# Optimization experiments

Hardware: AMD Instinct MI355X
Metric: run time of the kernel (lower is better)

## Reference

```python
import jax, jax.numpy as jnp
import numpy as np

L, H, W, C = 5, 32, 128, 256
HEADS, DH = 8, 32
NUM_TYPES, NUM_REL = 2, 4
INNER = HEADS * DH  # 256
LN_EPS = 1e-5


def setup_inputs() -> dict:
    key = jax.random.key(0)
    ks = jax.random.split(key, 16)
    s = 0.05
    x = jax.random.normal(ks[0], (L, H, W, C), jnp.float32)
    mask = jax.random.randint(ks[1], (H, W, 1, L), 0, 2).astype(jnp.int32)
    types = jax.random.randint(ks[2], (L,), 0, NUM_TYPES)
    # prior_encoding carries the node type in channel 2 (constant across H,W)
    prior_encoding = jnp.zeros((L, H, W, 3), jnp.float32)
    prior_encoding = prior_encoding.at[:, :, :, 2].set(
        jnp.broadcast_to(types[:, None, None].astype(jnp.float32), (L, H, W)))
    return {
        'x': x,
        'mask': mask,
        'prior_encoding': prior_encoding,
        'ln_gamma': jnp.ones((C,), jnp.float32),
        'ln_beta': jnp.zeros((C,), jnp.float32),
        'q_weight': jax.random.normal(ks[3], (NUM_TYPES, INNER, C), jnp.float32) * s,
        'q_bias': jnp.zeros((NUM_TYPES, INNER), jnp.float32),
        'k_weight': jax.random.normal(ks[4], (NUM_TYPES, INNER, C), jnp.float32) * s,
        'k_bias': jnp.zeros((NUM_TYPES, INNER), jnp.float32),
        'v_weight': jax.random.normal(ks[5], (NUM_TYPES, INNER, C), jnp.float32) * s,
        'v_bias': jnp.zeros((NUM_TYPES, INNER), jnp.float32),
        'a_weight': jax.random.normal(ks[6], (NUM_TYPES, C, INNER), jnp.float32) * s,
        'a_bias': jnp.zeros((NUM_TYPES, C), jnp.float32),
        'relation_att': jax.random.normal(ks[7], (NUM_REL, HEADS, DH, DH), jnp.float32) * s,
        'relation_msg': jax.random.normal(ks[8], (NUM_REL, HEADS, DH, DH), jnp.float32) * s,
    }


def reference(x, mask, prior_encoding, ln_gamma, ln_beta,
              q_weight, q_bias, k_weight, k_bias, v_weight, v_bias,
              a_weight, a_bias, relation_att, relation_msg):
    # --- prenorm (LayerNorm over last dim), x: (L,H,W,C) ---
    mu = jnp.mean(x, axis=-1, keepdims=True)
    var = jnp.mean(jnp.square(x - mu), axis=-1, keepdims=True)
    xn = (x - mu) * jax.lax.rsqrt(var + LN_EPS) * ln_gamma + ln_beta

    xh = jnp.transpose(xn, (1, 2, 0, 3))  # (H,W,L,C)
    types = prior_encoding[:, 0, 0, 2].astype(jnp.int32)
    types = jnp.clip(types, 0, None)  # (L,)
    n_types = q_weight.shape[0]
    heads, dh = relation_att.shape[1], relation_att.shape[2]
    Hh, Ww, Ll = xh.shape[0], xh.shape[1], xh.shape[2]

    def type_linear(w, b):  # per-token typed projection
        return jnp.einsum('hwlc,lic->hwli', xh, w[types]) + b[types]

    def to_heads(t):  # (H,W,L,inner) -> (m,H,W,L,dh)
        return jnp.transpose(t.reshape(Hh, Ww, Ll, heads, dh), (3, 0, 1, 2, 4))

    q = to_heads(type_linear(q_weight, q_bias))
    k = to_heads(type_linear(k_weight, k_bias))
    v = to_heads(type_linear(v_weight, v_bias))

    # per-edge relation matrices: rel_idx (L,L)
    rel_idx = types[:, None] * n_types + types[None, :]
    w_att = jnp.transpose(relation_att[rel_idx], (2, 0, 1, 3, 4))  # (m,L,L,dh,dh)
    w_msg = jnp.transpose(relation_msg[rel_idx], (2, 0, 1, 3, 4))  # (m,L,L,dh,dh)

    scale = jnp.asarray(dh, jnp.float32) ** -0.5
    # att_map = (q @ w_att) @ k^T, per (head, h, w, i, j)
    att = jnp.einsum('mhwip,mijpq,mhwjq->mhwij', q, w_att, k) * scale
    att = jnp.where(mask[None] == 0, jnp.float32(-1e9), att)  # mask: (1,H,W,1,L)
    att = jax.nn.softmax(att, axis=-1)

    # out = att @ (w_msg @ v)
    out = jnp.einsum('mhwij,mijpc,mhwjp->mhwic', att, w_msg, v)  # (m,H,W,L,dh)
    out = jnp.transpose(out, (1, 2, 3, 0, 4)).reshape(Hh, Ww, Ll, heads * dh)

    # typed output projection back to C
    out = jnp.einsum('hwli,lci->hwlc', out, a_weight[types]) + a_bias[types]
    return jnp.transpose(out, (2, 0, 1, 3))  # (L,H,W,C)
```

## Files before the change

### kernel.cpp

```cpp
#include <hip/hip_runtime.h>
#include <math.h>

#define LL 5
#define HH 32
#define WW 128
#define CC 256
#define HEADS 8
#define DHH 32
#define HW (HH*WW)
#define NTOK (LL*HW)
#define LN_EPS 1e-5f

typedef short bf16x8 __attribute__((ext_vector_type(8)));
typedef float f32x4 __attribute__((ext_vector_type(4)));
typedef unsigned short u16x8 __attribute__((ext_vector_type(8)));

__device__ __forceinline__ int clamp01(int t) { return t < 0 ? 0 : (t > 1 ? 1 : t); }

__device__ __forceinline__ unsigned short f2b(float f) {
    union { float f; unsigned u; } v; v.f = f;
    unsigned r = v.u + 0x7FFFu + ((v.u >> 16) & 1u);
    return (unsigned short)(r >> 16);
}
__device__ __forceinline__ float b2f(unsigned short u) {
    union { unsigned u; float f; } v; v.u = ((unsigned)u) << 16; return v.f;
}

__device__ __forceinline__ size_t frag_off(int row, int col) {
    return ((size_t)((row >> 4) * 8 + (col >> 5)) << 9)
         + (((col & 31) >> 3) << 7) + ((row & 15) << 3) + (col & 7);
}

__global__ __launch_bounds__(256) void setup_kernel(
        const float* __restrict__ x, const float* __restrict__ g, const float* __restrict__ b,
        unsigned short* __restrict__ xn,
        const float* __restrict__ qw, const float* __restrict__ aw,
        unsigned short* __restrict__ qwb, unsigned short* __restrict__ awb,
        const float* __restrict__ relA, const float* __restrict__ relM,
        const float* __restrict__ kw, const float* __restrict__ vw,
        const float* __restrict__ kb, const float* __restrict__ vb,
        unsigned short* __restrict__ wattb, unsigned short* __restrict__ wmsgb,
        float* __restrict__ batt, float* __restrict__ bmsg) {
    __shared__ float Bl[32][256];
    int blk = blockIdx.x;
    int wave = threadIdx.x >> 6, lane = threadIdx.x & 63;
    if (blk < 1280) {
        float4 gv = *(const float4*)(g + lane * 4);
        float4 bv = *(const float4*)(b + lane * 4);
        #pragma unroll
        for (int rr = 0; rr < 4; ++rr) {
            int row = blk * 16 + wave * 4 + rr;
            const float4 xv = *(const float4*)(x + (size_t)row * CC + lane * 4);
            float s1 = xv.x + xv.y + xv.z + xv.w;
            float s2 = xv.x * xv.x + xv.y * xv.y + xv.z * xv.z + xv.w * xv.w;
            #pragma unroll
            for (int off = 32; off; off >>= 1) {
                s1 += __shfl_xor(s1, off, 64);
                s2 += __shfl_xor(s2, off, 64);
            }
            float mu = s1 * (1.0f / CC);
            float inv = rsqrtf(s2 * (1.0f / CC) - mu * mu + LN_EPS);
            ushort4 o;
            o.x = f2b((xv.x - mu) * inv * gv.x + bv.x);
            o.y = f2b((xv.y - mu) * inv * gv.y + bv.y);
            o.z = f2b((xv.z - mu) * inv * gv.z + bv.z);
            o.w = f2b((xv.w - mu) * inv * gv.w + bv.w);
            *(ushort4*)(xn + frag_off(row, lane << 2)) = o;
        }
    } else if (blk < 1408) {
        int task = (blk - 1280) * 4 + wave;
        int mtx = task >> 8, rem = task & 255;
        int t = rem >> 7, panel = (rem >> 3) & 15, kk = rem & 7;
        const float* S = (mtx ? aw : qw) + (size_t)t * 65536
                       + (size_t)(panel * 16 + (lane & 15)) * 256 + kk * 32 + (lane >> 4) * 8;
        float4 f0 = *(const float4*)S;
        float4 f1 = *(const float4*)(S + 4);
        u16x8 o;
        o[0] = f2b(f0.x); o[1] = f2b(f0.y); o[2] = f2b(f0.z); o[3] = f2b(f0.w);
        o[4] = f2b(f1.x); o[5] = f2b(f1.y); o[6] = f2b(f1.z); o[7] = f2b(f1.w);
        unsigned short* D = (mtx ? awb : qwb) + (size_t)t * 65536
                          + (((size_t)(panel * 8 + kk)) << 9) + (lane << 3);
        *(u16x8*)D = o;
    } else {
        int fb = blk - 1408;
        int r = fb & 3, m = (fb >> 2) & 7, which = fb >> 5;
        int tsel = r & 1;
        const float* S  = (which ? relM : relA) + ((size_t)r * 8 + m) * 1024;
        const float* Bg = (which ? vw : kw) + (size_t)tsel * 65536 + (size_t)m * 32 * 256;
        const float* bv = (which ? vb : kb) + tsel * 256 + m * 32;
        unsigned short* Wf = (which ? wmsgb : wattb) + (size_t)r * 65536;
        float* bo = (which ? bmsg : batt) + r * 256 + m * 32;

        for (int i = threadIdx.x; i < 32 * 256; i += 256)
            Bl[i >> 8][i & 255] = Bg[(size_t)(i >> 8) * 256 + (i & 255)];
        __syncthreads();

        int a  = threadIdx.x >> 3;
        int c0 = (threadIdx.x & 7) * 4;
        float srow[32];
        #pragma unroll
        for (int bq = 0; bq < 32; ++bq)
            srow[bq] = which ? S[bq * 32 + a] : S[a * 32 + bq];
        float acc[8][4] = {{0.f}};
        #pragma unroll
        for (int bq = 0; bq < 32; ++bq) {
            float s = srow[bq];
            #pragma unroll
            for (int cc = 0; cc < 8; ++cc) {
                float4 bb = *(const float4*)&Bl[bq][c0 + cc * 32];
                acc[cc][0] += s * bb.x; acc[cc][1] += s * bb.y;
                acc[cc][2] += s * bb.z; acc[cc][3] += s * bb.w;
            }
        }
        int colpanel = m * 2 + (a >> 4);
        int jr = a & 15;
        #pragma unroll
        for (int cc = 0; cc < 8; ++cc) {
            ushort4 w4;
            w4.x = f2b(acc[cc][0]); w4.y = f2b(acc[cc][1]);
            w4.z = f2b(acc[cc][2]); w4.w = f2b(acc[cc][3]);
            *(ushort4*)(Wf + (((size_t)(colpanel * 8 + cc)) << 9)
                           + ((c0 >> 3) << 7) + (jr << 3) + (c0 & 7)) = w4;
        }
        if (threadIdx.x < 32) {
            int p = threadIdx.x;
            float s = 0.f;
            #pragma unroll
            for (int bq = 0; bq < 32; ++bq)
                s += (which ? S[bq * 32 + p] : S[p * 32 + bq]) * bv[bq];
            bo[p] = s;
        }
    }
}

__global__ __launch_bounds__(256) void gemm_qkv(const short* __restrict__ X,
        const short* __restrict__ qwb, const short* __restrict__ wattb,
        const short* __restrict__ wmsgb,
        const float* __restrict__ qb, const float* __restrict__ batt,
        const float* __restrict__ bmsg,
        const float* __restrict__ prior, unsigned short* __restrict__ OutBase) {
    __shared__ float R[4][16][68];
    int blkrow = blockIdx.x * 32;
    int s = blockIdx.y;
    int l = blkrow >> 12;
    int t = clamp01((int)prior[(size_t)l * HW * 3 + 2]);

    const short* Wp; const float* Bp;
    if (s == 0)      { Wp = qwb   + (size_t)t * 65536;                          Bp = qb   + t * 256; }
    else if (s <= 2) { int i2 = (s - 1) * 2 + t; Wp = wattb + (size_t)i2 * 65536; Bp = batt + i2 * 256; }
    else             { int i2 = (s - 3) * 2 + t; Wp = wmsgb + (size_t)i2 * 65536; Bp = bmsg + i2 * 256; }
    unsigned short* Out = OutBase + (size_t)s * NTOK * 256;

    int wave = threadIdx.x >> 6, lane = threadIdx.x & 63;
    int lr = lane & 15;
    const short* Xf = X + ((size_t)blockIdx.x << 13);

    f32x4 acc[2][4];
    #pragma unroll
    for (int mr = 0; mr < 2; ++mr)
        #pragma unroll
        for (int nr = 0; nr < 4; ++nr) acc[mr][nr] = (f32x4){0.f, 0.f, 0.f, 0.f};

    #pragma unroll
    for (int kk = 0; kk < 8; ++kk) {
        bf16x8 af[2], bf[4];
        #pragma unroll
        for (int mr = 0; mr < 2; ++mr)
            af[mr] = *(const bf16x8*)(Xf + (((size_t)(mr * 8 + kk)) << 9) + (lane << 3));
        #pragma unroll
        for (int nr = 0; nr < 4; ++nr)
            bf[nr] = *(const bf16x8*)(Wp + (((size_t)((wave * 4 + nr) * 8 + kk)) << 9) + (lane << 3));
        #pragma unroll
        for (int mr = 0; mr < 2; ++mr)
            #pragma unroll
            for (int nr = 0; nr < 4; ++nr)
                acc[mr][nr] = __builtin_amdgcn_mfma_f32_16x16x32_bf16(af[mr], bf[nr], acc[mr][nr], 0, 0, 0);
    }

    float bias[4];
    #pragma unroll
    for (int nr = 0; nr < 4; ++nr) bias[nr] = Bp[wave * 64 + nr * 16 + lr];

    int q = lane >> 4;
    int c8 = lane & 7;
    #pragma unroll
    for (int mr = 0; mr < 2; ++mr) {
        #pragma unroll
        for (int nr = 0; nr < 4; ++nr)
            #pragma unroll
            for (int rr = 0; rr < 4; ++rr)
                R[wave][q * 4 + rr][nr * 16 + lr] = acc[mr][nr][rr] + bias[nr];
        #pragma unroll
        for (int p = 0; p < 2; ++p) {
            int r = (lane >> 3) + p * 8;
            float4 v0 = *(const float4*)&R[wave][r][c8 * 8];
            float4 v1 = *(const float4*)&R[wave][r][c8 * 8 + 4];
            u16x8 w;
            w[0] = f2b(v0.x); w[1] = f2b(v0.y); w[2] = f2b(v0.z); w[3] = f2b(v0.w);
            w[4] = f2b(v1.x); w[5] = f2b(v1.y); w[6] = f2b(v1.z); w[7] = f2b(v1.w);
            *(u16x8*)(Out + (size_t)(blkrow + mr * 16 + r) * 256 + wave * 64 + c8 * 8) = w;
        }
        __builtin_amdgcn_wave_barrier();
    }
}

__global__ __launch_bounds__(256) void attn_proj(
        const unsigned short* __restrict__ QKV, const short* __restrict__ awb,
        const float* __restrict__ ab, const int* __restrict__ mask,
        const float* __restrict__ prior, float* __restrict__ out) {
    __shared__ unsigned short Att[32 * 256];
    const size_t TSTR = (size_t)NTOK * 256;
    int tid = threadIdx.x;
    int blkrow = blockIdx.x * 32;
    int i = blkrow >> 12;
    int t = clamp01((int)prior[(size_t)i * HW * 3 + 2]);

    int tok = tid >> 3, m = tid & 7;
    int row = blkrow + tok;
    int hw = row & (HW - 1);

    {
        const unsigned short* Qp = QKV + (size_t)row * 256 + m * 32;
        const unsigned short* Kb = QKV + (size_t)(1 + t) * TSTR + (size_t)hw * 256 + m * 32;
        const unsigned short* Vb = QKV + (size_t)(3 + t) * TSTR + (size_t)hw * 256 + m * 32;

        float qf[32];
        #pragma unroll
        for (int c = 0; c < 4; ++c) {
            bf16x8 qv = *(const bf16x8*)(Qp + c * 8);
            #pragma unroll
            for (int e = 0; e < 8; ++e) qf[c * 8 + e] = b2f((unsigned short)qv[e]);
        }

        const float scale = 0.17677669529663687f;
        float s[LL];
        #pragma unroll
        for (int j = 0; j < LL; ++j) {
            const unsigned short* Kp = Kb + (size_t)j * HW * 256;
            float acc = 0.f;
            #pragma unroll
            for (int c = 0; c < 4; ++c) {
                bf16x8 kv = *(const bf16x8*)(Kp + c * 8);
                #pragma unroll
                for (int e = 0; e < 8; ++e)
                    acc = fmaf(qf[c * 8 + e], b2f((unsigned short)kv[e]), acc);
            }
            int mk = mask[hw * LL + j];
            s[j] = mk ? acc * scale : -1e9f;
        }

        float mx = fmaxf(fmaxf(fmaxf(s[0], s[1]), fmaxf(s[2], s[3])), s[4]);
        float e5[LL], sum = 0.f;
        #pragma unroll
        for (int j = 0; j < LL; ++j) { e5[j] = __expf(s[j] - mx); sum += e5[j]; }
        float inv = 1.f / sum;

        float o[32];
        #pragma unroll
        for (int c = 0; c < 32; ++c) o[c] = 0.f;
        #pragma unroll
        for (int j = 0; j < LL; ++j) {
            const unsigned short* Vp = Vb + (size_t)j * HW * 256;
            float ej = e5[j];
            #pragma unroll
            for (int c = 0; c < 4; ++c) {
                bf16x8 vv = *(const bf16x8*)(Vp + c * 8);
                #pragma unroll
                for (int e = 0; e < 8; ++e)
                    o[c * 8 + e] = fmaf(ej, b2f((unsigned short)vv[e]), o[c * 8 + e]);
            }
        }

        int panel = tok >> 4, tr = tok & 15;
        #pragma unroll
        for (int c8 = 0; c8 < 4; ++c8) {
            u16x8 w;
            #pragma unroll
            for (int e = 0; e < 8; ++e) w[e] = f2b(o[c8 * 8 + e] * inv);
            *(u16x8*)(&Att[((panel * 8 + m) << 9) + c8 * 128 + tr * 8]) = w;
        }
    }
    __syncthreads();

    int wave = tid >> 6, lane = tid & 63, lr = lane & 15;
    const short* Wp = awb + (size_t)t * 65536;
    const float* Bp = ab + (size_t)t * 256;

    f32x4 acc[2][4];
    #pragma unroll
    for (int mr = 0; mr < 2; ++mr)
        #pragma unroll
        for (int nr = 0; nr < 4; ++nr) acc[mr][nr] = (f32x4){0.f, 0.f, 0.f, 0.f};

    #pragma unroll
    for (int kk = 0; kk < 8; ++kk) {
        bf16x8 af[2], bf[4];
        #pragma unroll
        for (int mr = 0; mr < 2; ++mr)
            af[mr] = *(const bf16x8*)((const short*)Att + ((mr * 8 + kk) << 9) + (lane << 3));
        #pragma unroll
        for (int nr = 0; nr < 4; ++nr)
            bf[nr] = *(const bf16x8*)(Wp + (((size_t)((wave * 4 + nr) * 8 + kk)) << 9) + (lane << 3));
        #pragma unroll
        for (int mr = 0; mr < 2; ++mr)
            #pragma unroll
            for (int nr = 0; nr < 4; ++nr)
                acc[mr][nr] = __builtin_amdgcn_mfma_f32_16x16x32_bf16(af[mr], bf[nr], acc[mr][nr], 0, 0, 0);
    }

    #pragma unroll
    for (int nr = 0; nr < 4; ++nr) {
        int col = wave * 64 + nr * 16 + lr;
        float bias = Bp[col];
        #pragma unroll
        for (int mr = 0; mr < 2; ++mr) {
            #pragma unroll
            for (int rr = 0; rr < 4; ++rr) {
                int orow = blkrow + mr * 16 + (lane >> 4) * 4 + rr;
                out[(size_t)orow * 256 + col] = acc[mr][nr][rr] + bias;
            }
        }
    }
}

extern "C" void kernel_launch(void* const* d_in, const int* in_sizes, int n_in,
                              void* d_out, int out_size, void* d_ws, size_t ws_size,
                              hipStream_t stream) {
    (void)in_sizes; (void)n_in; (void)out_size; (void)ws_size;
    const float* x     = (const float*)d_in[0];
    const int*   mask  = (const int*)d_in[1];
    const float* prior = (const float*)d_in[2];
    const float* ln_g  = (const float*)d_in[3];
    const float* ln_b  = (const float*)d_in[4];
    const float* qw    = (const float*)d_in[5];
    const float* qb    = (const float*)d_in[6];
    const float* kw    = (const float*)d_in[7];
    const float* kb    = (const float*)d_in[8];
    const float* vw    = (const float*)d_in[9];
    const float* vb    = (const float*)d_in[10];
    const float* aw    = (const float*)d_in[11];
    const float* ab    = (const float*)d_in[12];
    const float* relA  = (const float*)d_in[13];
    const float* relM  = (const float*)d_in[14];
    float* out = (float*)d_out;

    char* ws = (char*)d_ws;
    const size_t TOKB = (size_t)NTOK * 256 * 2;
    unsigned short* xnb  = (unsigned short*)(ws);
    unsigned short* Qb   = (unsigned short*)(ws + TOKB);
    char* wsp = ws + 6 * TOKB;
    unsigned short* qwb   = (unsigned short*)(wsp);            wsp += 131072 * 2;
    unsigned short* awb   = (unsigned short*)(wsp);            wsp += 131072 * 2;
    unsigned short* wattb = (unsigned short*)(wsp);            wsp += 4 * 65536 * 2;
    unsigned short* wmsgb = (unsigned short*)(wsp);            wsp += 4 * 65536 * 2;
    float* batt = (float*)(wsp);                               wsp += 4 * 256 * 4;
    float* bmsg = (float*)(wsp);

    setup_kernel<<<1472, 256, 0, stream>>>(x, ln_g, ln_b, xnb, qw, aw, qwb, awb,
                                           relA, relM, kw, vw, kb, vb,
                                           wattb, wmsgb, batt, bmsg);

    gemm_qkv<<<dim3(NTOK / 32, 5), 256, 0, stream>>>((const short*)xnb,
            (const short*)qwb, (const short*)wattb, (const short*)wmsgb,
            qb, batt, bmsg, prior, Qb);

    attn_proj<<<NTOK / 32, 256, 0, stream>>>(Qb, (const short*)awb, ab, mask, prior, out);
}
```

Before: 64.49 us.

## Keep weight fragments in registers and loop over eight row panels per block

The QKV GEMM kernel now loads its 64-column weight slice into registers once per wave and reuses it across eight 16-row panels, instead of reloading weights for every 32-row block. The grid shrinks from 640 to 160 blocks per projection, and launch bounds request two blocks per SIMD. This is meant to cut repeated weight traffic from L2 and the per-block setup cost. In exchange it uses many more VGPRs for the 32 held weight fragments, which may cause spills, and the smaller grid (800 blocks total) lowers parallelism.

```diff
diff --git a/kernel.cpp b/kernel.cpp
--- a/kernel.cpp
+++ b/kernel.cpp
@@ -133,16 +133,18 @@
     }
 }
 
-__global__ __launch_bounds__(256) void gemm_qkv(const short* __restrict__ X,
+__global__ __launch_bounds__(256, 2) void gemm_qkv(const short* __restrict__ X,
         const short* __restrict__ qwb, const short* __restrict__ wattb,
         const short* __restrict__ wmsgb,
         const float* __restrict__ qb, const float* __restrict__ batt,
         const float* __restrict__ bmsg,
         const float* __restrict__ prior, unsigned short* __restrict__ OutBase) {
     __shared__ float R[4][16][68];
-    int blkrow = blockIdx.x * 32;
+    int chunk = blockIdx.x;
+    int l = chunk >> 5;
+    int base_panel = l * 256 + (chunk & 31) * 8;
+    int base_row = base_panel << 4;
     int s = blockIdx.y;
-    int l = blkrow >> 12;
     int t = clamp01((int)prior[(size_t)l * HW * 3 + 2]);
 
     const short* Wp; const float* Bp;
@@ -153,29 +155,13 @@
 
     int wave = threadIdx.x >> 6, lane = threadIdx.x & 63;
     int lr = lane & 15;
-    const short* Xf = X + ((size_t)blockIdx.x << 13);
-
-    f32x4 acc[2][4];
-    #pragma unroll
-    for (int mr = 0; mr < 2; ++mr)
-        #pragma unroll
-        for (int nr = 0; nr < 4; ++nr) acc[mr][nr] = (f32x4){0.f, 0.f, 0.f, 0.f};
-
-    #pragma unroll
-    for (int kk = 0; kk < 8; ++kk) {
-        bf16x8 af[2], bf[4];
-        #pragma unroll
-        for (int mr = 0; mr < 2; ++mr)
-            af[mr] = *(const bf16x8*)(Xf + (((size_t)(mr * 8 + kk)) << 9) + (lane << 3));
-        #pragma unroll
-        for (int nr = 0; nr < 4; ++nr)
-            bf[nr] = *(const bf16x8*)(Wp + (((size_t)((wave * 4 + nr) * 8 + kk)) << 9) + (lane << 3));
-        #pragma unroll
-        for (int mr = 0; mr < 2; ++mr)
-            #pragma unroll
-            for (int nr = 0; nr < 4; ++nr)
-                acc[mr][nr] = __builtin_amdgcn_mfma_f32_16x16x32_bf16(af[mr], bf[nr], acc[mr][nr], 0, 0, 0);
-    }
+
+    bf16x8 bf[4][8];
+    #pragma unroll
+    for (int nr = 0; nr < 4; ++nr)
+        #pragma unroll
+        for (int kk = 0; kk < 8; ++kk)
+            bf[nr][kk] = *(const bf16x8*)(Wp + (((size_t)((wave * 4 + nr) * 8 + kk)) << 9) + (lane << 3));
 
     float bias[4];
     #pragma unroll
@@ -183,22 +169,37 @@
 
     int q = lane >> 4;
     int c8 = lane & 7;
-    #pragma unroll
-    for (int mr = 0; mr < 2; ++mr) {
+
+    for (int p = 0; p < 8; ++p) {
+        const short* Ap = X + (((size_t)(base_panel + p)) << 12);
+        bf16x8 af[8];
+        #pragma unroll
+        for (int kk = 0; kk < 8; ++kk)
+            af[kk] = *(const bf16x8*)(Ap + (kk << 9) + (lane << 3));
+
+        f32x4 acc[4];
+        #pragma unroll
+        for (int nr = 0; nr < 4; ++nr) acc[nr] = (f32x4){0.f, 0.f, 0.f, 0.f};
+        #pragma unroll
+        for (int kk = 0; kk < 8; ++kk)
+            #pragma unroll
+            for (int nr = 0; nr < 4; ++nr)
+                acc[nr] = __builtin_amdgcn_mfma_f32_16x16x32_bf16(af[kk], bf[nr][kk], acc[nr], 0, 0, 0);
+
         #pragma unroll
         for (int nr = 0; nr < 4; ++nr)
             #pragma unroll
             for (int rr = 0; rr < 4; ++rr)
-                R[wave][q * 4 + rr][nr * 16 + lr] = acc[mr][nr][rr] + bias[nr];
-        #pragma unroll
-        for (int p = 0; p < 2; ++p) {
-            int r = (lane >> 3) + p * 8;
+                R[wave][q * 4 + rr][nr * 16 + lr] = acc[nr][rr] + bias[nr];
+        #pragma unroll
+        for (int ph = 0; ph < 2; ++ph) {
+            int r = (lane >> 3) + ph * 8;
             float4 v0 = *(const float4*)&R[wave][r][c8 * 8];
             float4 v1 = *(const float4*)&R[wave][r][c8 * 8 + 4];
             u16x8 w;
             w[0] = f2b(v0.x); w[1] = f2b(v0.y); w[2] = f2b(v0.z); w[3] = f2b(v0.w);
             w[4] = f2b(v1.x); w[5] = f2b(v1.y); w[6] = f2b(v1.z); w[7] = f2b(v1.w);
-            *(u16x8*)(Out + (size_t)(blkrow + mr * 16 + r) * 256 + wave * 64 + c8 * 8) = w;
+            *(u16x8*)(Out + (size_t)(base_row + p * 16 + r) * 256 + wave * 64 + c8 * 8) = w;
         }
         __builtin_amdgcn_wave_barrier();
     }
@@ -360,7 +361,7 @@
                                            relA, relM, kw, vw, kb, vb,
                                            wattb, wmsgb, batt, bmsg);
 
-    gemm_qkv<<<dim3(NTOK / 32, 5), 256, 0, stream>>>((const short*)xnb,
+    gemm_qkv<<<dim3(160, 5), 256, 0, stream>>>((const short*)xnb,
             (const short*)qwb, (const short*)wattb, (const short*)wmsgb,
             qb, batt, bmsg, prior, Qb);
 
```

New measurement: 78.10 us. 21.1% more time.

## Split QKV GEMM column halves across blocks and halve attn_proj tile rows

Applied to the files above, without the earlier changes.

The QKV GEMM grid doubles in y so each block computes only half of the 256 output columns, which cuts per-wave accumulators and the staging buffer. The attention/projection kernel now handles 16 tokens per block with 128 threads, and each of its two waves covers 128 output columns. Both changes raise block count and occupancy and lower register pressure. The cost is that X tiles are reloaded twice in the GEMM and each projection weight tile is reused across fewer rows.

```diff
diff --git a/kernel.cpp b/kernel.cpp
--- a/kernel.cpp
+++ b/kernel.cpp
@@ -139,9 +139,9 @@
         const float* __restrict__ qb, const float* __restrict__ batt,
         const float* __restrict__ bmsg,
         const float* __restrict__ prior, unsigned short* __restrict__ OutBase) {
-    __shared__ float R[4][16][68];
+    __shared__ float R[4][16][36];
     int blkrow = blockIdx.x * 32;
-    int s = blockIdx.y;
+    int s = blockIdx.y >> 1, nh = blockIdx.y & 1;
     int l = blkrow >> 12;
     int t = clamp01((int)prior[(size_t)l * HW * 3 + 2]);
 
@@ -154,64 +154,61 @@
     int wave = threadIdx.x >> 6, lane = threadIdx.x & 63;
     int lr = lane & 15;
     const short* Xf = X + ((size_t)blockIdx.x << 13);
-
-    f32x4 acc[2][4];
+    int cpb = nh * 8 + wave * 2;
+
+    f32x4 acc[2][2];
     #pragma unroll
     for (int mr = 0; mr < 2; ++mr)
         #pragma unroll
-        for (int nr = 0; nr < 4; ++nr) acc[mr][nr] = (f32x4){0.f, 0.f, 0.f, 0.f};
+        for (int nr = 0; nr < 2; ++nr) acc[mr][nr] = (f32x4){0.f, 0.f, 0.f, 0.f};
 
     #pragma unroll
     for (int kk = 0; kk < 8; ++kk) {
-        bf16x8 af[2], bf[4];
+        bf16x8 af[2], bf[2];
         #pragma unroll
         for (int mr = 0; mr < 2; ++mr)
             af[mr] = *(const bf16x8*)(Xf + (((size_t)(mr * 8 + kk)) << 9) + (lane << 3));
         #pragma unroll
-        for (int nr = 0; nr < 4; ++nr)
-            bf[nr] = *(const bf16x8*)(Wp + (((size_t)((wave * 4 + nr) * 8 + kk)) << 9) + (lane << 3));
+        for (int nr = 0; nr < 2; ++nr)
+            bf[nr] = *(const bf16x8*)(Wp + (((size_t)((cpb + nr) * 8 + kk)) << 9) + (lane << 3));
         #pragma unroll
         for (int mr = 0; mr < 2; ++mr)
             #pragma unroll
-            for (int nr = 0; nr < 4; ++nr)
+            for (int nr = 0; nr < 2; ++nr)
                 acc[mr][nr] = __builtin_amdgcn_mfma_f32_16x16x32_bf16(af[mr], bf[nr], acc[mr][nr], 0, 0, 0);
     }
 
-    float bias[4];
-    #pragma unroll
-    for (int nr = 0; nr < 4; ++nr) bias[nr] = Bp[wave * 64 + nr * 16 + lr];
+    float bias[2];
+    #pragma unroll
+    for (int nr = 0; nr < 2; ++nr) bias[nr] = Bp[nh * 128 + wave * 32 + nr * 16 + lr];
 
     int q = lane >> 4;
-    int c8 = lane & 7;
     #pragma unroll
     for (int mr = 0; mr < 2; ++mr) {
         #pragma unroll
-        for (int nr = 0; nr < 4; ++nr)
+        for (int nr = 0; nr < 2; ++nr)
             #pragma unroll
             for (int rr = 0; rr < 4; ++rr)
                 R[wave][q * 4 + rr][nr * 16 + lr] = acc[mr][nr][rr] + bias[nr];
-        #pragma unroll
-        for (int p = 0; p < 2; ++p) {
-            int r = (lane >> 3) + p * 8;
-            float4 v0 = *(const float4*)&R[wave][r][c8 * 8];
-            float4 v1 = *(const float4*)&R[wave][r][c8 * 8 + 4];
-            u16x8 w;
-            w[0] = f2b(v0.x); w[1] = f2b(v0.y); w[2] = f2b(v0.z); w[3] = f2b(v0.w);
-            w[4] = f2b(v1.x); w[5] = f2b(v1.y); w[6] = f2b(v1.z); w[7] = f2b(v1.w);
-            *(u16x8*)(Out + (size_t)(blkrow + mr * 16 + r) * 256 + wave * 64 + c8 * 8) = w;
-        }
+        int r = lane >> 2, c8 = lane & 3;
+        float4 v0 = *(const float4*)&R[wave][r][c8 * 8];
+        float4 v1 = *(const float4*)&R[wave][r][c8 * 8 + 4];
+        u16x8 w;
+        w[0] = f2b(v0.x); w[1] = f2b(v0.y); w[2] = f2b(v0.z); w[3] = f2b(v0.w);
+        w[4] = f2b(v1.x); w[5] = f2b(v1.y); w[6] = f2b(v1.z); w[7] = f2b(v1.w);
+        *(u16x8*)(Out + (size_t)(blkrow + mr * 16 + r) * 256 + nh * 128 + wave * 32 + c8 * 8) = w;
         __builtin_amdgcn_wave_barrier();
     }
 }
 
-__global__ __launch_bounds__(256) void attn_proj(
+__global__ __launch_bounds__(128) void attn_proj(
         const unsigned short* __restrict__ QKV, const short* __restrict__ awb,
         const float* __restrict__ ab, const int* __restrict__ mask,
         const float* __restrict__ prior, float* __restrict__ out) {
-    __shared__ unsigned short Att[32 * 256];
+    __shared__ unsigned short Att[16 * 256];
     const size_t TSTR = (size_t)NTOK * 256;
     int tid = threadIdx.x;
-    int blkrow = blockIdx.x * 32;
+    int blkrow = blockIdx.x * 16;
     int i = blkrow >> 12;
     int t = clamp01((int)prior[(size_t)i * HW * 3 + 2]);
 
@@ -271,13 +268,12 @@
             }
         }
 
-        int panel = tok >> 4, tr = tok & 15;
         #pragma unroll
         for (int c8 = 0; c8 < 4; ++c8) {
             u16x8 w;
             #pragma unroll
             for (int e = 0; e < 8; ++e) w[e] = f2b(o[c8 * 8 + e] * inv);
-            *(u16x8*)(&Att[((panel * 8 + m) << 9) + c8 * 128 + tr * 8]) = w;
+            *(u16x8*)(&Att[(m << 9) + c8 * 128 + tok * 8]) = w;
         }
     }
     __syncthreads();
@@ -286,39 +282,28 @@
     const short* Wp = awb + (size_t)t * 65536;
     const float* Bp = ab + (size_t)t * 256;
 
-    f32x4 acc[2][4];
-    #pragma unroll
-    for (int mr = 0; mr < 2; ++mr)
-        #pragma unroll
-        for (int nr = 0; nr < 4; ++nr) acc[mr][nr] = (f32x4){0.f, 0.f, 0.f, 0.f};
+    f32x4 acc[8];
+    #pragma unroll
+    for (int nr = 0; nr < 8; ++nr) acc[nr] = (f32x4){0.f, 0.f, 0.f, 0.f};
 
     #pragma unroll
     for (int kk = 0; kk < 8; ++kk) {
-        bf16x8 af[2], bf[4];
-        #pragma unroll
-        for (int mr = 0; mr < 2; ++mr)
-            af[mr] = *(const bf16x8*)((const short*)Att + ((mr * 8 + kk) << 9) + (lane << 3));
-        #pragma unroll
-        for (int nr = 0; nr < 4; ++nr)
-            bf[nr] = *(const bf16x8*)(Wp + (((size_t)((wave * 4 + nr) * 8 + kk)) << 9) + (lane << 3));
-        #pragma unroll
-        for (int mr = 0; mr < 2; ++mr)
-            #pragma unroll
-            for (int nr = 0; nr < 4; ++nr)
-                acc[mr][nr] = __builtin_amdgcn_mfma_f32_16x16x32_bf16(af[mr], bf[nr], acc[mr][nr], 0, 0, 0);
-    }
-
-    #pragma unroll
-    for (int nr = 0; nr < 4; ++nr) {
-        int col = wave * 64 + nr * 16 + lr;
+        bf16x8 af = *(const bf16x8*)((const short*)Att + (kk << 9) + (lane << 3));
+        #pragma unroll
+        for (int nr = 0; nr < 8; ++nr) {
+            bf16x8 bf = *(const bf16x8*)(Wp + (((size_t)((wave * 8 + nr) * 8 + kk)) << 9) + (lane << 3));
+            acc[nr] = __builtin_amdgcn_mfma_f32_16x16x32_bf16(af, bf, acc[nr], 0, 0, 0);
+        }
+    }
+
+    #pragma unroll
+    for (int nr = 0; nr < 8; ++nr) {
+        int col = wave * 128 + nr * 16 + lr;
         float bias = Bp[col];
         #pragma unroll
-        for (int mr = 0; mr < 2; ++mr) {
-            #pragma unroll
-            for (int rr = 0; rr < 4; ++rr) {
-                int orow = blkrow + mr * 16 + (lane >> 4) * 4 + rr;
-                out[(size_t)orow * 256 + col] = acc[mr][nr][rr] + bias;
-            }
+        for (int rr = 0; rr < 4; ++rr) {
+            int orow = blkrow + (lane >> 4) * 4 + rr;
+            out[(size_t)orow * 256 + col] = acc[nr][rr] + bias;
         }
     }
 }
@@ -360,9 +345,9 @@
                                            relA, relM, kw, vw, kb, vb,
                                            wattb, wmsgb, batt, bmsg);
 
-    gemm_qkv<<<dim3(NTOK / 32, 5), 256, 0, stream>>>((const short*)xnb,
+    gemm_qkv<<<dim3(640, 10), 256, 0, stream>>>((const short*)xnb,
             (const short*)qwb, (const short*)wattb, (const short*)wmsgb,
             qb, batt, bmsg, prior, Qb);
 
-    attn_proj<<<NTOK / 32, 256, 0, stream>>>(Qb, (const short*)awb, ab, mask, prior, out);
-}
+    attn_proj<<<NTOK / 16, 128, 0, stream>>>(Qb, (const short*)awb, ab, mask, prior, out);
+}
```

Result: slower. 67.84 us (+5.2%).
